# Kernel tuning notes

Measured on AMD Instinct MI355X. Metric: run time of the kernel, lower is better.

## Reference

```python
import jax, jax.numpy as jnp
import numpy as np

NEG_SLOPE = 0.2  # PyG GATv2Conv default negative_slope


def _gatv2_layer(x, src, dst, Wl, Wr, att, bias, heads, out_ch, concat, num_nodes):
    # x: [N, F_in]; src/dst: [E'] (self-loops already appended)
    N, H, C = num_nodes, heads, out_ch
    xl = (x @ Wl).reshape(N, H, C)  # source-side transform (lin_l)
    xr = (x @ Wr).reshape(N, H, C)  # target-side transform (lin_r)
    m = xl[src] + xr[dst]                       # [E', H, C]
    e = jax.nn.leaky_relu(m, NEG_SLOPE)
    logits = jnp.einsum('ehc,hc->eh', e, att)   # [E', H]
    # numerically stable segment softmax over incoming edges of each dst node
    mx = jax.ops.segment_max(logits, dst, num_segments=N)   # [N, H]
    ex = jnp.exp(logits - mx[dst])
    den = jax.ops.segment_sum(ex, dst, num_segments=N)      # [N, H]
    alpha = ex / den[dst]                                    # [E', H]
    out = jax.ops.segment_sum(alpha[:, :, None] * xl[src], dst, num_segments=N)  # [N, H, C]
    out = out.reshape(N, H * C) if concat else out.mean(axis=1)
    return out + bias


def setup_inputs() -> dict:
    key = jax.random.key(0)
    N, E = 50000, 800000
    IN, HID, OUT, HEADS = 128, 32, 64, 4
    ks = jax.random.split(key, 16)
    x = jax.random.normal(ks[0], (N, IN), dtype=jnp.float32)
    edge_index = jax.random.randint(ks[1], (2, E), 0, N, dtype=jnp.int64)

    def lin(k, fin, fout):
        return jax.random.normal(k, (fin, fout), dtype=jnp.float32) * (1.0 / np.sqrt(fin))

    HC = HID * HEADS  # 128
    inp = {
        'x': x, 'edge_index': edge_index,
        # layer 1: IN -> HID x HEADS, concat
        'Wl1': lin(ks[2], IN, HC), 'Wr1': lin(ks[3], IN, HC),
        'a1': jax.random.normal(ks[4], (HEADS, HID), dtype=jnp.float32) * 0.1,
        'b1': jnp.zeros((HC,), dtype=jnp.float32),
        # layer 2: HC -> HID x HEADS, concat
        'Wl2': lin(ks[5], HC, HC), 'Wr2': lin(ks[6], HC, HC),
        'a2': jax.random.normal(ks[7], (HEADS, HID), dtype=jnp.float32) * 0.1,
        'b2': jnp.zeros((HC,), dtype=jnp.float32),
        # layer 3: HC -> OUT, heads=1, concat=False
        'Wl3': lin(ks[8], HC, OUT), 'Wr3': lin(ks[9], HC, OUT),
        'a3': jax.random.normal(ks[10], (1, OUT), dtype=jnp.float32) * 0.1,
        'b3': jnp.zeros((OUT,), dtype=jnp.float32),
    }
    return inp


def reference(x, edge_index, Wl1, Wr1, a1, b1, Wl2, Wr2, a2, b2, Wl3, Wr3, a3, b3):
    N = x.shape[0]
    # PyG GATv2Conv default add_self_loops=True
    loops = jnp.arange(N, dtype=edge_index.dtype)
    src = jnp.concatenate([edge_index[0], loops])
    dst = jnp.concatenate([edge_index[1], loops])
    HID, HEADS, OUT = 32, 4, 64
    h = _gatv2_layer(x, src, dst, Wl1, Wr1, a1, b1, HEADS, HID, True, N)
    h = jax.nn.elu(h)  # eval mode: dropout is identity
    h = _gatv2_layer(h, src, dst, Wl2, Wr2, a2, b2, HEADS, HID, True, N)
    h = jax.nn.elu(h)
    out = _gatv2_layer(h, src, dst, Wl3, Wr3, a3, b3, 1, OUT, False, N)
    return out
```

## Files before the change

kernel.cpp:

```cpp
#include <hip/hip_runtime.h>
#include <cstdint>
#include <cstddef>
#include <math.h>

#define NEG_SLOPE 0.2f
#define DEGB 512
#define EB 4096

typedef unsigned short ushort_t;
typedef __attribute__((ext_vector_type(8))) short short8;
typedef __attribute__((ext_vector_type(4))) float f32x4;
typedef _Float16 half8 __attribute__((ext_vector_type(8)));
typedef _Float16 half2_t __attribute__((ext_vector_type(2)));

__device__ __forceinline__ ushort_t f2bf(float f) {
    unsigned u = __float_as_uint(f);
    unsigned r = u + 0x7FFFu + ((u >> 16) & 1u);
    return (ushort_t)(r >> 16);
}
__device__ __forceinline__ float bf2f(ushort_t h) {
    return __uint_as_float(((unsigned)h) << 16);
}
__device__ __forceinline__ ushort_t f2h(float f) {
    _Float16 h = (_Float16)f;
    return *(ushort_t*)&h;
}

__device__ __forceinline__ float dot2acc(half2_t a, half2_t b, float c) {
#if __has_builtin(__builtin_amdgcn_fdot2)
    return __builtin_amdgcn_fdot2(a, b, c, false);
#else
    return c + (float)a[0] * (float)b[0] + (float)a[1] * (float)b[1];
#endif
}

template<int CTRL>
__device__ __forceinline__ float dpp_add(float p) {
    int t = __builtin_amdgcn_update_dpp(0, __builtin_bit_cast(int, p),
                                        CTRL, 0xF, 0xF, true);
    return p + __builtin_bit_cast(float, t);
}

__device__ __forceinline__ float swz4_add(float p) {
    int t = __builtin_amdgcn_ds_swizzle(__builtin_bit_cast(int, p), 0x101F);
    return p + __builtin_bit_cast(float, t);
}

__device__ __forceinline__ int wave_incl_scan(int v, int lane) {
    #pragma unroll
    for (int o = 1; o < 64; o <<= 1) {
        int t = __shfl_up(v, o, 64);
        if (lane >= o) v += t;
    }
    return v;
}


__global__ void bucket_hist(const int* __restrict__ ei, int E, int Et,
                            int* __restrict__ blkcnt) {
    __shared__ int cnt[256];
    int t = threadIdx.x;
    cnt[t] = 0;
    __syncthreads();
    int e0 = blockIdx.x * EB;
    #pragma unroll
    for (int it = 0; it < EB / 256; ++it) {
        int e = e0 + it * 256 + t;
        if (e < Et) {
            int d = (e < E) ? ei[E + e] : (e - E);
            atomicAdd(&cnt[d >> 8], 1);
        }
    }
    __syncthreads();
    blkcnt[blockIdx.x * 256 + t] = cnt[t];
}

__global__ void colscan(int* __restrict__ blkcnt, int nblk, int* __restrict__ btot) {
    int b = blockIdx.x;
    int lane = threadIdx.x;
    int running = 0;
    for (int base = 0; base < nblk; base += 64) {
        int idx = base + lane;
        int v = (idx < nblk) ? blkcnt[idx * 256 + b] : 0;
        int incl = wave_incl_scan(v, lane);
        if (idx < nblk) blkcnt[idx * 256 + b] = running + incl - v;
        running += __shfl(incl, 63, 64);
    }
    if (lane == 0) btot[b] = running;
}

__global__ void bucketscan(const int* __restrict__ btot, int* __restrict__ bbase) {
    __shared__ int tmp[256];
    int t = threadIdx.x;
    int v = btot[t];
    tmp[t] = v;
    __syncthreads();
    for (int o = 1; o < 256; o <<= 1) {
        int x = (t >= o) ? tmp[t - o] : 0;
        __syncthreads();
        tmp[t] += x;
        __syncthreads();
    }
    bbase[t] = tmp[t] - v;
}

__global__ void bucket_scatter(const int* __restrict__ ei, int E, int Et,
                               const int* __restrict__ blkrel,
                               const int* __restrict__ bbase,
                               unsigned* __restrict__ ebuf) {
    __shared__ int base_l[256];
    __shared__ int cnt[256];
    int t = threadIdx.x;
    base_l[t] = bbase[t] + blkrel[blockIdx.x * 256 + t];
    cnt[t] = 0;
    __syncthreads();
    int e0 = blockIdx.x * EB;
    #pragma unroll
    for (int it = 0; it < EB / 256; ++it) {
        int e = e0 + it * 256 + t;
        if (e < Et) {
            int s, d;
            if (e < E) { s = ei[e]; d = ei[E + e]; }
            else       { s = d = e - E; }
            int b = d >> 8;
            int r = atomicAdd(&cnt[b], 1);
            ebuf[base_l[b] + r] = (unsigned)s | (((unsigned)d & 255u) << 17);
        }
    }
}

__global__ void csr_count(const unsigned* __restrict__ ebuf,
                          const int* __restrict__ bbase,
                          const int* __restrict__ btot,
                          int N, int* __restrict__ deg) {
    __shared__ int dcnt[256];
    int b = blockIdx.x, t = threadIdx.x;
    dcnt[t] = 0;
    __syncthreads();
    int s0 = bbase[b], c = btot[b];
    for (int i = t; i < c; i += 256)
        atomicAdd(&dcnt[ebuf[s0 + i] >> 17], 1);
    __syncthreads();
    int node = b * 256 + t;
    if (node < N) deg[node] = dcnt[t];
}

__global__ void csr_scatter2(const unsigned* __restrict__ ebuf,
                             const int* __restrict__ bbase,
                             const int* __restrict__ btot,
                             const int* __restrict__ rowstart,
                             int N, int* __restrict__ csr_src) {
    __shared__ int cur[256];
    int b = blockIdx.x, t = threadIdx.x;
    int node = b * 256 + t;
    cur[t] = (node < N) ? rowstart[node] : 0;
    __syncthreads();
    int s0 = bbase[b], c = btot[b];
    for (int i = t; i < c; i += 256) {
        unsigned v = ebuf[s0 + i];
        int pos = atomicAdd(&cur[v >> 17], 1);
        csr_src[pos] = (int)(v & 0x1FFFFu);
    }
}

__global__ void scan1(const int* __restrict__ deg, int N,
                      int* __restrict__ excl, int* __restrict__ partials) {
    __shared__ int tmp[256];
    int i = blockIdx.x * 256 + threadIdx.x;
    int v = (i < N) ? deg[i] : 0;
    tmp[threadIdx.x] = v;
    __syncthreads();
    for (int o = 1; o < 256; o <<= 1) {
        int t = (threadIdx.x >= (unsigned)o) ? tmp[threadIdx.x - o] : 0;
        __syncthreads();
        tmp[threadIdx.x] += t;
        __syncthreads();
    }
    if (i < N) excl[i] = tmp[threadIdx.x] - v;
    if (threadIdx.x == 255) partials[blockIdx.x] = tmp[255];
}

__global__ void scan23(int* __restrict__ excl, const int* __restrict__ partials,
                       int nb, int N, int* __restrict__ cursor) {
    __shared__ int tmp[256];
    int t = threadIdx.x;
    tmp[t] = (t < nb) ? partials[t] : 0;
    __syncthreads();
    for (int o = 1; o < 256; o <<= 1) {
        int x = (t >= o) ? tmp[t - o] : 0;
        __syncthreads();
        tmp[t] += x;
        __syncthreads();
    }
    int off = (blockIdx.x > 0) ? tmp[blockIdx.x - 1] : 0;
    int i = blockIdx.x * 256 + t;
    if (i < N) {
        int v = excl[i] + off;
        excl[i] = v;
        cursor[i] = v;
    }
}

__global__ void deg_hist_blk(const int* __restrict__ deg, int N,
                             int* __restrict__ dhist) {
    __shared__ int h[DEGB];
    int t = threadIdx.x;
    for (int b = t; b < DEGB; b += 256) h[b] = 0;
    __syncthreads();
    int i = blockIdx.x * 256 + t;
    if (i < N) {
        int d = deg[i]; if (d > DEGB - 1) d = DEGB - 1;
        atomicAdd(&h[d], 1);
    }
    __syncthreads();
    for (int b = t; b < DEGB; b += 256) {
        int c = h[b];
        if (c) atomicAdd(&dhist[b], c);
    }
}
__global__ void deg_scan(const int* __restrict__ dhist, int* __restrict__ dstart) {
    __shared__ int tmp[DEGB];
    int t = threadIdx.x;
    tmp[t] = dhist[t];
    __syncthreads();
    for (int o = 1; o < DEGB; o <<= 1) {
        int v = (t >= o) ? tmp[t - o] : 0;
        __syncthreads();
        tmp[t] += v;
        __syncthreads();
    }
    int total = tmp[DEGB - 1];
    dstart[t] = total - tmp[t];
}
__global__ void deg_scatter_blk(const int* __restrict__ deg, int N,
                                int* __restrict__ dstart, int* __restrict__ perm) {
    __shared__ int h[DEGB];
    __shared__ int base[DEGB];
    int t = threadIdx.x;
    for (int b = t; b < DEGB; b += 256) h[b] = 0;
    __syncthreads();
    int i = blockIdx.x * 256 + t;
    int d = 0, r = 0;
    if (i < N) {
        d = deg[i]; if (d > DEGB - 1) d = DEGB - 1;
        r = atomicAdd(&h[d], 1);
    }
    __syncthreads();
    for (int b = t; b < DEGB; b += 256) {
        int c = h[b];
        if (c) base[b] = atomicAdd(&dstart[b], c);
    }
    __syncthreads();
    if (i < N) perm[base[d] + r] = i;
}

template<int MOUT, bool CONVA>
__global__ __launch_bounds__(256) void gemm_mfma(const ushort_t* __restrict__ Ah,
                                                 const ushort_t* __restrict__ Al,
                                                 const float* __restrict__ Af,
                                                 const float* __restrict__ Wl,
                                                 const float* __restrict__ Wr,
                                                 ushort_t* __restrict__ xlh,
                                                 ushort_t* __restrict__ xrh, int N) {
    __shared__ __align__(16) ushort_t Bh[8192];
    __shared__ __align__(16) ushort_t Bl[8192];
    const int tid   = threadIdx.x;
    const int row0  = blockIdx.x * 128;
    const int col0v = blockIdx.y * 64;
    const bool isR  = col0v >= MOUT;
    const float* W  = isR ? Wr : Wl;
    const int wcol0 = isR ? (col0v - MOUT) : col0v;
    ushort_t* OUT   = isR ? xrh : xlh;

    #pragma unroll
    for (int i = 0; i < 8; ++i) {
        int idx = tid * 8 + i;
        int k   = idx >> 4;
        int c4  = (idx & 15) * 4;
        float4 w = *(const float4*)(W + (size_t)k * MOUT + wcol0 + c4);
        float wv[4] = {w.x, w.y, w.z, w.w};
        int q = k >> 5, quad = (k >> 3) & 3, j = k & 7;
        #pragma unroll
        for (int e = 0; e < 4; ++e) {
            int c = c4 + e;
            int t = c >> 4;
            int l = (quad << 4) | (c & 15);
            int pos = ((t * 4 + q) * 64 + l) * 8 + j;
            ushort_t hb = f2bf(wv[e]);
            Bh[pos] = hb;
            Bl[pos] = f2bf(wv[e] - bf2f(hb));
        }
    }
    __syncthreads();

    const int wv_  = tid >> 6;
    const int lane = tid & 63;
    const int m    = lane & 15;
    const int quad = lane >> 4;
    const int wrow0 = row0 + wv_ * 32;

    f32x4 acc[2][4] = {};

    for (int q = 0; q < 4; ++q) {
        short8 ahf[2], alf[2];
        #pragma unroll
        for (int r = 0; r < 2; ++r) {
            int row = wrow0 + 16 * r + m;
            row = row < N ? row : N - 1;
            size_t off = (size_t)row * 128 + q * 32 + quad * 8;
            if constexpr (CONVA) {
                float4 f0 = *(const float4*)(Af + off);
                float4 f1 = *(const float4*)(Af + off + 4);
                float fv[8] = {f0.x, f0.y, f0.z, f0.w, f1.x, f1.y, f1.z, f1.w};
                short ah[8], al[8];
                #pragma unroll
                for (int e = 0; e < 8; ++e) {
                    ushort_t hb = f2bf(fv[e]);
                    ah[e] = (short)hb;
                    al[e] = (short)f2bf(fv[e] - bf2f(hb));
                }
                ahf[r] = short8{ah[0],ah[1],ah[2],ah[3],ah[4],ah[5],ah[6],ah[7]};
                alf[r] = short8{al[0],al[1],al[2],al[3],al[4],al[5],al[6],al[7]};
            } else {
                ahf[r] = *(const short8*)(Ah + off);
                alf[r] = *(const short8*)(Al + off);
            }
        }
        #pragma unroll
        for (int t = 0; t < 4; ++t) {
            int base = ((t * 4 + q) * 64 + lane) * 8;
            short8 bh = *(const short8*)(Bh + base);
            short8 bl = *(const short8*)(Bl + base);
            #pragma unroll
            for (int r = 0; r < 2; ++r) {
                acc[r][t] = __builtin_amdgcn_mfma_f32_16x16x32_bf16(ahf[r], bh, acc[r][t], 0, 0, 0);
                acc[r][t] = __builtin_amdgcn_mfma_f32_16x16x32_bf16(ahf[r], bl, acc[r][t], 0, 0, 0);
                acc[r][t] = __builtin_amdgcn_mfma_f32_16x16x32_bf16(alf[r], bh, acc[r][t], 0, 0, 0);
            }
        }
    }

    #pragma unroll
    for (int r = 0; r < 2; ++r)
        #pragma unroll
        for (int i = 0; i < 4; ++i) {
            int row = wrow0 + 16 * r + quad * 4 + i;
            if (row < N) {
                #pragma unroll
                for (int t = 0; t < 4; ++t)
                    OUT[(size_t)row * MOUT + wcol0 + t * 16 + m] = f2h(acc[r][t][i]);
            }
        }
}

template<int H, int C, bool ELU, int OMODE>
__global__ __launch_bounds__(512) void node_attn(const ushort_t* __restrict__ xlh,
                                                 const ushort_t* __restrict__ xrh,
                                                 const float* __restrict__ att,
                                                 const float* __restrict__ bias,
                                                 const int* __restrict__ rowstart,
                                                 const int* __restrict__ deg,
                                                 const int* __restrict__ csr_src,
                                                 const int* __restrict__ perm,
                                                 int N, float* __restrict__ out,
                                                 ushort_t* __restrict__ outh,
                                                 ushort_t* __restrict__ outl) {
    constexpr int HC  = H * C;
    constexpr int VPT = 8;
    constexpr int LPG = HC / VPT;
    constexpr int GPW = 64 / LPG;
    constexpr int GROUP = C / VPT;
    constexpr int DR  = 5;

    const int lane = threadIdx.x & 63;
    const int wv   = threadIdx.x >> 6;
    const int gid  = lane / LPG;
    const int lig  = lane % LPG;
    const int ch0  = lig * VPT;

    const int g0      = (blockIdx.x * 8 + wv) * GPW + gid;
    const int gstride = gridDim.x * 8 * GPW;

    half2_t a2[4];
    {
        float4 u0 = *(const float4*)(att + ch0);
        float4 u1 = *(const float4*)(att + ch0 + 4);
        a2[0] = half2_t{(_Float16)u0.x, (_Float16)u0.y};
        a2[1] = half2_t{(_Float16)u0.z, (_Float16)u0.w};
        a2[2] = half2_t{(_Float16)u1.x, (_Float16)u1.y};
        a2[3] = half2_t{(_Float16)u1.z, (_Float16)u1.w};
    }
    float bias8[VPT];
    {
        float4 b0 = *(const float4*)(bias + ch0);
        float4 b1 = *(const float4*)(bias + ch0 + 4);
        bias8[0]=b0.x; bias8[1]=b0.y; bias8[2]=b0.z; bias8[3]=b0.w;
        bias8[4]=b1.x; bias8[5]=b1.y; bias8[6]=b1.z; bias8[7]=b1.w;
    }
    const half2_t c02 = half2_t{(_Float16)NEG_SLOPE, (_Float16)NEG_SLOPE};

    for (int s = g0; s < N; s += gstride) {
        const int n  = perm[s];
        const int j0 = rowstart[n];
        const int dg = deg[n];

        half8 xrv = *(const half8*)(xrh + (size_t)n * HC + ch0);

        auto ldidx = [&](int e) {
            int ee = e < dg ? e : dg - 1;
            return csr_src[j0 + ee];
        };
        auto ldrow = [&](int idx) -> half8 {
            return *(const half8*)(xlh + (size_t)(unsigned)idx * HC + ch0);
        };

        float d = 0.f;
        float acc[VPT] = {};

        auto process = [&](half8 v) {
            float p = 0.f;
            #pragma unroll
            for (int i = 0; i < 4; ++i) {
                half2_t v2 = half2_t{v[2 * i], v[2 * i + 1]};
                half2_t x2 = half2_t{xrv[2 * i], xrv[2 * i + 1]};
                half2_t m2 = v2 + x2;
                half2_t lr = __builtin_elementwise_max(m2, c02 * m2);
                p = dot2acc(lr, a2[i], p);
            }
            if constexpr (GROUP >= 2) p = dpp_add<0xB1>(p);
            if constexpr (GROUP >= 4) p = dpp_add<0x4E>(p);
            if constexpr (GROUP >= 8) p = swz4_add(p);
            float pe = __expf(p);
            d += pe;
            #pragma unroll
            for (int i = 0; i < VPT; ++i)
                acc[i] += pe * (float)v[i];
        };

        int   ibuf[DR];
        half8 rbuf[DR];
        #pragma unroll
        for (int k = 0; k < DR; ++k) ibuf[k] = ldidx(k);
        #pragma unroll
        for (int k = 0; k < DR; ++k) {
            rbuf[k] = ldrow(ibuf[k]);
            ibuf[k] = ldidx(k + DR);
        }

        int e = 0;
        for (; e + DR <= dg; e += DR) {
            #pragma unroll
            for (int k = 0; k < DR; ++k) {
                half8 v = rbuf[k];
                rbuf[k] = ldrow(ibuf[k]);
                ibuf[k] = ldidx(e + k + 2 * DR);
                process(v);
            }
        }
        #pragma unroll
        for (int k = 0; k < DR; ++k)
            if (e + k < dg) process(rbuf[k]);

        float inv = 1.f / d;
        float vv[VPT];
        #pragma unroll
        for (int i = 0; i < VPT; ++i) {
            float v = acc[i] * inv + bias8[i];
            if (ELU) v = v > 0.f ? v : (__expf(v) - 1.f);
            vv[i] = v;
        }
        if (OMODE == 0) {
            *(float4*)(out + (size_t)n * HC + ch0) =
                make_float4(vv[0], vv[1], vv[2], vv[3]);
            *(float4*)(out + (size_t)n * HC + ch0 + 4) =
                make_float4(vv[4], vv[5], vv[6], vv[7]);
        } else {
            ushort_t hb[VPT], lb[VPT];
            #pragma unroll
            for (int i = 0; i < VPT; ++i) {
                hb[i] = f2bf(vv[i]);
                lb[i] = f2bf(vv[i] - bf2f(hb[i]));
            }
            *(ushort4*)(outh + (size_t)n * HC + ch0) =
                ushort4{hb[0], hb[1], hb[2], hb[3]};
            *(ushort4*)(outh + (size_t)n * HC + ch0 + 4) =
                ushort4{hb[4], hb[5], hb[6], hb[7]};
            *(ushort4*)(outl + (size_t)n * HC + ch0) =
                ushort4{lb[0], lb[1], lb[2], lb[3]};
            *(ushort4*)(outl + (size_t)n * HC + ch0 + 4) =
                ushort4{lb[4], lb[5], lb[6], lb[7]};
        }
    }
}

extern "C" void kernel_launch(void* const* d_in, const int* in_sizes, int n_in,
                              void* d_out, int out_size, void* d_ws, size_t ws_size,
                              hipStream_t stream) {
    const float* x   = (const float*)d_in[0];
    const int*   ei  = (const int*)d_in[1];
    const float* Wl1 = (const float*)d_in[2];
    const float* Wr1 = (const float*)d_in[3];
    const float* a1  = (const float*)d_in[4];
    const float* b1  = (const float*)d_in[5];
    const float* Wl2 = (const float*)d_in[6];
    const float* Wr2 = (const float*)d_in[7];
    const float* a2  = (const float*)d_in[8];
    const float* b2  = (const float*)d_in[9];
    const float* Wl3 = (const float*)d_in[10];
    const float* Wr3 = (const float*)d_in[11];
    const float* a3  = (const float*)d_in[12];
    const float* b3  = (const float*)d_in[13];

    const int N  = in_sizes[0] / 128;
    const int E  = in_sizes[1] / 2;
    const int Et = E + N;
    const int nb = (N + 255) / 256;

    char* p = (char*)d_ws;
    auto alloc = [&](size_t bytes) -> void* {
        void* r = (void*)p;
        p += (bytes + 255) & ~(size_t)255;
        return r;
    };
    const int ebBlocks = (Et + EB - 1) / EB;
    int*      csr_src  = (int*)alloc((size_t)Et * 4 + 256);
    unsigned* ebuf     = (unsigned*)alloc((size_t)Et * 4);
    int*      blkcnt   = (int*)alloc((size_t)ebBlocks * 256 * 4);
    int*      btot     = (int*)alloc(256 * 4);
    int*      bbase    = (int*)alloc(256 * 4);
    int*      deg      = (int*)alloc((size_t)N * 4);
    int*      rowstart = (int*)alloc((size_t)N * 4);
    int*      cursor   = (int*)alloc((size_t)N * 4);
    int*      partials = (int*)alloc((size_t)nb * 4);
    int*      perm     = (int*)alloc((size_t)N * 4);
    int*      dhist    = (int*)alloc((size_t)DEGB * 4);
    int*      dstart   = (int*)alloc((size_t)DEGB * 4);
    ushort_t* xlh      = (ushort_t*)alloc((size_t)N * 128 * 2);
    ushort_t* xrh      = (ushort_t*)alloc((size_t)N * 128 * 2);
    ushort_t* Ah       = (ushort_t*)alloc((size_t)N * 128 * 2);
    ushort_t* Al       = (ushort_t*)alloc((size_t)N * 128 * 2);

    const int rowBlocks   = (N + 127) / 128;
    const int nodeBlocks12 = (N + 31) / 32;
    const int nodeBlocks3  = (N + 63) / 64;

    hipMemsetAsync(dhist, 0, (size_t)DEGB * 4, stream);
    bucket_hist<<<ebBlocks, 256, 0, stream>>>(ei, E, Et, blkcnt);
    colscan<<<256, 64, 0, stream>>>(blkcnt, ebBlocks, btot);
    bucketscan<<<1, 256, 0, stream>>>(btot, bbase);
    bucket_scatter<<<ebBlocks, 256, 0, stream>>>(ei, E, Et, blkcnt, bbase, ebuf);
    csr_count<<<nb, 256, 0, stream>>>(ebuf, bbase, btot, N, deg);
    scan1<<<nb, 256, 0, stream>>>(deg, N, rowstart, partials);
    scan23<<<nb, 256, 0, stream>>>(rowstart, partials, nb, N, cursor);
    csr_scatter2<<<nb, 256, 0, stream>>>(ebuf, bbase, btot, rowstart, N, csr_src);
    deg_hist_blk<<<nb, 256, 0, stream>>>(deg, N, dhist);
    deg_scan<<<1, DEGB, 0, stream>>>(dhist, dstart);
    deg_scatter_blk<<<nb, 256, 0, stream>>>(deg, N, dstart, perm);

    gemm_mfma<128, true><<<dim3(rowBlocks, 4), 256, 0, stream>>>(
        nullptr, nullptr, x, Wl1, Wr1, xlh, xrh, N);
    node_attn<4, 32, true, 1><<<nodeBlocks12, 512, 0, stream>>>(
        xlh, xrh, a1, b1, rowstart, deg, csr_src, perm, N, nullptr, Ah, Al);

    gemm_mfma<128, false><<<dim3(rowBlocks, 4), 256, 0, stream>>>(
        Ah, Al, nullptr, Wl2, Wr2, xlh, xrh, N);
    node_attn<4, 32, true, 1><<<nodeBlocks12, 512, 0, stream>>>(
        xlh, xrh, a2, b2, rowstart, deg, csr_src, perm, N, nullptr, Ah, Al);

    float* out = (float*)d_out;
    gemm_mfma<64, false><<<dim3(rowBlocks, 2), 256, 0, stream>>>(
        Ah, Al, nullptr, Wl3, Wr3, xlh, xrh, N);
    node_attn<1, 64, false, 0><<<nodeBlocks3, 512, 0, stream>>>(
        xlh, xrh, a3, b3, rowstart, deg, csr_src, perm, N, out, nullptr, nullptr);
}
```

Measured before the change: 309.5 us.

## Fuse CSR and degree-sort preprocessing into one persistent kernel with grid barriers

Eleven small preprocessing kernels (bucket histogram, scans, scatters, CSR count and scatter, degree sort) are merged into a single kernel that uses atomic-counter grid barriers between phases. Count, scan, and degree-histogram steps now share one phase, and the unused cursor buffer is dropped. The aim is to remove per-launch overhead and the gaps between many tiny dependent kernels. The cost is that correctness depends on all blocks (ebBlocks, about 208 with 256 threads) being co-resident, or the spin barrier deadlocks, and phases where few blocks have work now block the whole grid.

```diff
diff --git a/kernel.cpp b/kernel.cpp
--- a/kernel.cpp
+++ b/kernel.cpp
@@ -56,202 +56,183 @@
 }
 
 
-__global__ void bucket_hist(const int* __restrict__ ei, int E, int Et,
-                            int* __restrict__ blkcnt) {
-    __shared__ int cnt[256];
-    int t = threadIdx.x;
-    cnt[t] = 0;
+__device__ __forceinline__ void gbar(int* __restrict__ bar, int ph, int nblk) {
     __syncthreads();
-    int e0 = blockIdx.x * EB;
-    #pragma unroll
-    for (int it = 0; it < EB / 256; ++it) {
-        int e = e0 + it * 256 + t;
-        if (e < Et) {
-            int d = (e < E) ? ei[E + e] : (e - E);
-            atomicAdd(&cnt[d >> 8], 1);
-        }
+    if (threadIdx.x == 0) {
+        __threadfence();
+        atomicAdd(&bar[ph], 1);
+        while (__hip_atomic_load(&bar[ph], __ATOMIC_RELAXED,
+                                 __HIP_MEMORY_SCOPE_AGENT) < nblk) {}
     }
     __syncthreads();
-    blkcnt[blockIdx.x * 256 + t] = cnt[t];
-}
-
-__global__ void colscan(int* __restrict__ blkcnt, int nblk, int* __restrict__ btot) {
-    int b = blockIdx.x;
-    int lane = threadIdx.x;
-    int running = 0;
-    for (int base = 0; base < nblk; base += 64) {
-        int idx = base + lane;
-        int v = (idx < nblk) ? blkcnt[idx * 256 + b] : 0;
-        int incl = wave_incl_scan(v, lane);
-        if (idx < nblk) blkcnt[idx * 256 + b] = running + incl - v;
-        running += __shfl(incl, 63, 64);
-    }
-    if (lane == 0) btot[b] = running;
-}
-
-__global__ void bucketscan(const int* __restrict__ btot, int* __restrict__ bbase) {
-    __shared__ int tmp[256];
-    int t = threadIdx.x;
-    int v = btot[t];
-    tmp[t] = v;
+    __threadfence();
+}
+
+__global__ __launch_bounds__(256) void build_all(
+        const int* __restrict__ ei, int E, int Et, int N, int nbkt,
+        int* __restrict__ blkcnt, int* __restrict__ btot, int* __restrict__ bbase,
+        unsigned* __restrict__ ebuf,
+        int* __restrict__ deg, int* __restrict__ rowstart, int* __restrict__ partials,
+        int* __restrict__ dhist, int* __restrict__ dstart, int* __restrict__ perm,
+        int* __restrict__ csr_src, int* __restrict__ bar) {
+    __shared__ int sA[256];
+    __shared__ int sB[256];
+    __shared__ int sC[512];
+    __shared__ int sD[512];
+    const int t    = threadIdx.x;
+    const int blk  = blockIdx.x;
+    const int nblk = gridDim.x;
+
+    sA[t] = 0;
     __syncthreads();
-    for (int o = 1; o < 256; o <<= 1) {
-        int x = (t >= o) ? tmp[t - o] : 0;
-        __syncthreads();
-        tmp[t] += x;
-        __syncthreads();
-    }
-    bbase[t] = tmp[t] - v;
-}
-
-__global__ void bucket_scatter(const int* __restrict__ ei, int E, int Et,
-                               const int* __restrict__ blkrel,
-                               const int* __restrict__ bbase,
-                               unsigned* __restrict__ ebuf) {
-    __shared__ int base_l[256];
-    __shared__ int cnt[256];
-    int t = threadIdx.x;
-    base_l[t] = bbase[t] + blkrel[blockIdx.x * 256 + t];
-    cnt[t] = 0;
-    __syncthreads();
-    int e0 = blockIdx.x * EB;
-    #pragma unroll
-    for (int it = 0; it < EB / 256; ++it) {
-        int e = e0 + it * 256 + t;
-        if (e < Et) {
-            int s, d;
-            if (e < E) { s = ei[e]; d = ei[E + e]; }
-            else       { s = d = e - E; }
-            int b = d >> 8;
-            int r = atomicAdd(&cnt[b], 1);
-            ebuf[base_l[b] + r] = (unsigned)s | (((unsigned)d & 255u) << 17);
-        }
-    }
-}
-
-__global__ void csr_count(const unsigned* __restrict__ ebuf,
-                          const int* __restrict__ bbase,
-                          const int* __restrict__ btot,
-                          int N, int* __restrict__ deg) {
-    __shared__ int dcnt[256];
-    int b = blockIdx.x, t = threadIdx.x;
-    dcnt[t] = 0;
-    __syncthreads();
-    int s0 = bbase[b], c = btot[b];
-    for (int i = t; i < c; i += 256)
-        atomicAdd(&dcnt[ebuf[s0 + i] >> 17], 1);
-    __syncthreads();
-    int node = b * 256 + t;
-    if (node < N) deg[node] = dcnt[t];
-}
-
-__global__ void csr_scatter2(const unsigned* __restrict__ ebuf,
-                             const int* __restrict__ bbase,
-                             const int* __restrict__ btot,
-                             const int* __restrict__ rowstart,
-                             int N, int* __restrict__ csr_src) {
-    __shared__ int cur[256];
-    int b = blockIdx.x, t = threadIdx.x;
-    int node = b * 256 + t;
-    cur[t] = (node < N) ? rowstart[node] : 0;
-    __syncthreads();
-    int s0 = bbase[b], c = btot[b];
-    for (int i = t; i < c; i += 256) {
-        unsigned v = ebuf[s0 + i];
-        int pos = atomicAdd(&cur[v >> 17], 1);
-        csr_src[pos] = (int)(v & 0x1FFFFu);
-    }
-}
-
-__global__ void scan1(const int* __restrict__ deg, int N,
-                      int* __restrict__ excl, int* __restrict__ partials) {
-    __shared__ int tmp[256];
-    int i = blockIdx.x * 256 + threadIdx.x;
-    int v = (i < N) ? deg[i] : 0;
-    tmp[threadIdx.x] = v;
-    __syncthreads();
-    for (int o = 1; o < 256; o <<= 1) {
-        int t = (threadIdx.x >= (unsigned)o) ? tmp[threadIdx.x - o] : 0;
-        __syncthreads();
-        tmp[threadIdx.x] += t;
-        __syncthreads();
-    }
-    if (i < N) excl[i] = tmp[threadIdx.x] - v;
-    if (threadIdx.x == 255) partials[blockIdx.x] = tmp[255];
-}
-
-__global__ void scan23(int* __restrict__ excl, const int* __restrict__ partials,
-                       int nb, int N, int* __restrict__ cursor) {
-    __shared__ int tmp[256];
-    int t = threadIdx.x;
-    tmp[t] = (t < nb) ? partials[t] : 0;
-    __syncthreads();
-    for (int o = 1; o < 256; o <<= 1) {
-        int x = (t >= o) ? tmp[t - o] : 0;
-        __syncthreads();
-        tmp[t] += x;
-        __syncthreads();
-    }
-    int off = (blockIdx.x > 0) ? tmp[blockIdx.x - 1] : 0;
-    int i = blockIdx.x * 256 + t;
-    if (i < N) {
-        int v = excl[i] + off;
-        excl[i] = v;
-        cursor[i] = v;
-    }
-}
-
-__global__ void deg_hist_blk(const int* __restrict__ deg, int N,
-                             int* __restrict__ dhist) {
-    __shared__ int h[DEGB];
-    int t = threadIdx.x;
-    for (int b = t; b < DEGB; b += 256) h[b] = 0;
-    __syncthreads();
-    int i = blockIdx.x * 256 + t;
-    if (i < N) {
-        int d = deg[i]; if (d > DEGB - 1) d = DEGB - 1;
-        atomicAdd(&h[d], 1);
-    }
-    __syncthreads();
-    for (int b = t; b < DEGB; b += 256) {
-        int c = h[b];
-        if (c) atomicAdd(&dhist[b], c);
-    }
-}
-__global__ void deg_scan(const int* __restrict__ dhist, int* __restrict__ dstart) {
-    __shared__ int tmp[DEGB];
-    int t = threadIdx.x;
-    tmp[t] = dhist[t];
-    __syncthreads();
-    for (int o = 1; o < DEGB; o <<= 1) {
-        int v = (t >= o) ? tmp[t - o] : 0;
-        __syncthreads();
-        tmp[t] += v;
-        __syncthreads();
-    }
-    int total = tmp[DEGB - 1];
-    dstart[t] = total - tmp[t];
-}
-__global__ void deg_scatter_blk(const int* __restrict__ deg, int N,
-                                int* __restrict__ dstart, int* __restrict__ perm) {
-    __shared__ int h[DEGB];
-    __shared__ int base[DEGB];
-    int t = threadIdx.x;
-    for (int b = t; b < DEGB; b += 256) h[b] = 0;
-    __syncthreads();
-    int i = blockIdx.x * 256 + t;
-    int d = 0, r = 0;
-    if (i < N) {
-        d = deg[i]; if (d > DEGB - 1) d = DEGB - 1;
-        r = atomicAdd(&h[d], 1);
-    }
-    __syncthreads();
-    for (int b = t; b < DEGB; b += 256) {
-        int c = h[b];
-        if (c) base[b] = atomicAdd(&dstart[b], c);
-    }
-    __syncthreads();
-    if (i < N) perm[base[d] + r] = i;
+    {
+        int e0 = blk * EB;
+        #pragma unroll
+        for (int it = 0; it < EB / 256; ++it) {
+            int e = e0 + it * 256 + t;
+            if (e < Et) {
+                int d = (e < E) ? ei[E + e] : (e - E);
+                atomicAdd(&sA[d >> 8], 1);
+            }
+        }
+        __syncthreads();
+        blkcnt[blk * 256 + t] = sA[t];
+    }
+    gbar(bar, 0, nblk);
+
+    for (int b = blk; b < 256; b += nblk) {
+        if (t < 64) {
+            int lane = t;
+            int running = 0;
+            for (int base = 0; base < nblk; base += 64) {
+                int idx = base + lane;
+                int v = (idx < nblk) ? blkcnt[idx * 256 + b] : 0;
+                int incl = wave_incl_scan(v, lane);
+                if (idx < nblk) blkcnt[idx * 256 + b] = running + incl - v;
+                running += __shfl(incl, 63, 64);
+            }
+            if (lane == 0) btot[b] = running;
+        }
+    }
+    gbar(bar, 1, nblk);
+
+    if (blk == 0) {
+        int v = btot[t];
+        sB[t] = v;
+        __syncthreads();
+        for (int o = 1; o < 256; o <<= 1) {
+            int x = (t >= o) ? sB[t - o] : 0;
+            __syncthreads();
+            sB[t] += x;
+            __syncthreads();
+        }
+        bbase[t] = sB[t] - v;
+    }
+    gbar(bar, 2, nblk);
+
+    {
+        sA[t] = bbase[t] + blkcnt[blk * 256 + t];
+        sB[t] = 0;
+        __syncthreads();
+        int e0 = blk * EB;
+        #pragma unroll
+        for (int it = 0; it < EB / 256; ++it) {
+            int e = e0 + it * 256 + t;
+            if (e < Et) {
+                int s, d;
+                if (e < E) { s = ei[e]; d = ei[E + e]; }
+                else       { s = d = e - E; }
+                int b = d >> 8;
+                int r = atomicAdd(&sB[b], 1);
+                ebuf[sA[b] + r] = (unsigned)s | (((unsigned)d & 255u) << 17);
+            }
+        }
+    }
+    gbar(bar, 3, nblk);
+
+    int rs_excl = 0;
+    if (blk < nbkt) {
+        sA[t] = 0;
+        sC[t] = 0; sC[t + 256] = 0;
+        __syncthreads();
+        int s0 = bbase[blk], c = btot[blk];
+        for (int i = t; i < c; i += 256)
+            atomicAdd(&sA[ebuf[s0 + i] >> 17], 1);
+        __syncthreads();
+        int node = blk * 256 + t;
+        int dv = sA[t];
+        if (node < N) deg[node] = dv;
+        sB[t] = dv;
+        __syncthreads();
+        for (int o = 1; o < 256; o <<= 1) {
+            int x = (t >= o) ? sB[t - o] : 0;
+            __syncthreads();
+            sB[t] += x;
+            __syncthreads();
+        }
+        rs_excl = sB[t] - dv;
+        if (t == 255) partials[blk] = sB[255];
+        if (node < N) {
+            int dc = dv < DEGB - 1 ? dv : DEGB - 1;
+            atomicAdd(&sC[dc], 1);
+        }
+        __syncthreads();
+        int c0 = sC[t];       if (c0) atomicAdd(&dhist[t], c0);
+        int c1 = sC[t + 256]; if (c1) atomicAdd(&dhist[t + 256], c1);
+    }
+    gbar(bar, 4, nblk);
+
+    if (blk < nbkt) {
+        sB[t] = (t < nbkt) ? partials[t] : 0;
+        __syncthreads();
+        for (int o = 1; o < 256; o <<= 1) {
+            int x = (t >= o) ? sB[t - o] : 0;
+            __syncthreads();
+            sB[t] += x;
+            __syncthreads();
+        }
+        int off = (blk > 0) ? sB[blk - 1] : 0;
+        int node = blk * 256 + t;
+        if (node < N) rowstart[node] = rs_excl + off;
+    } else if (blk == nbkt) {
+        sC[t]       = dhist[t];
+        sC[t + 256] = dhist[t + 256];
+        __syncthreads();
+        for (int o = 1; o < 512; o <<= 1) {
+            int v0 = (t >= o) ? sC[t - o] : 0;
+            int v1 = (t + 256 >= o) ? sC[t + 256 - o] : 0;
+            __syncthreads();
+            sC[t] += v0;
+            sC[t + 256] += v1;
+            __syncthreads();
+        }
+        int total = sC[511];
+        dstart[t]       = total - sC[t];
+        dstart[t + 256] = total - sC[t + 256];
+    }
+    gbar(bar, 5, nblk);
+
+    if (blk < nbkt) {
+        int node = blk * 256 + t;
+        sB[t] = (node < N) ? rowstart[node] : 0;
+        sC[t] = 0; sC[t + 256] = 0;
+        __syncthreads();
+        int s0 = bbase[blk], c = btot[blk];
+        for (int i = t; i < c; i += 256) {
+            unsigned v = ebuf[s0 + i];
+            int pos = atomicAdd(&sB[v >> 17], 1);
+            csr_src[pos] = (int)(v & 0x1FFFFu);
+        }
+        int dv = sA[t];
+        int dc = dv < DEGB - 1 ? dv : DEGB - 1;
+        int r = 0;
+        if (node < N) r = atomicAdd(&sC[dc], 1);
+        __syncthreads();
+        int c0 = sC[t];       if (c0) sD[t]       = atomicAdd(&dstart[t], c0);
+        int c1 = sC[t + 256]; if (c1) sD[t + 256] = atomicAdd(&dstart[t + 256], c1);
+        __syncthreads();
+        if (node < N) perm[sD[dc] + r] = node;
+    }
 }
 
 template<int MOUT, bool CONVA>
@@ -530,10 +511,10 @@
     int*      bbase    = (int*)alloc(256 * 4);
     int*      deg      = (int*)alloc((size_t)N * 4);
     int*      rowstart = (int*)alloc((size_t)N * 4);
-    int*      cursor   = (int*)alloc((size_t)N * 4);
     int*      partials = (int*)alloc((size_t)nb * 4);
     int*      perm     = (int*)alloc((size_t)N * 4);
     int*      dhist    = (int*)alloc((size_t)DEGB * 4);
+    int*      bar      = (int*)alloc(64 * 4);
     int*      dstart   = (int*)alloc((size_t)DEGB * 4);
     ushort_t* xlh      = (ushort_t*)alloc((size_t)N * 128 * 2);
     ushort_t* xrh      = (ushort_t*)alloc((size_t)N * 128 * 2);
@@ -544,18 +525,10 @@
     const int nodeBlocks12 = (N + 31) / 32;
     const int nodeBlocks3  = (N + 63) / 64;
 
-    hipMemsetAsync(dhist, 0, (size_t)DEGB * 4, stream);
-    bucket_hist<<<ebBlocks, 256, 0, stream>>>(ei, E, Et, blkcnt);
-    colscan<<<256, 64, 0, stream>>>(blkcnt, ebBlocks, btot);
-    bucketscan<<<1, 256, 0, stream>>>(btot, bbase);
-    bucket_scatter<<<ebBlocks, 256, 0, stream>>>(ei, E, Et, blkcnt, bbase, ebuf);
-    csr_count<<<nb, 256, 0, stream>>>(ebuf, bbase, btot, N, deg);
-    scan1<<<nb, 256, 0, stream>>>(deg, N, rowstart, partials);
-    scan23<<<nb, 256, 0, stream>>>(rowstart, partials, nb, N, cursor);
-    csr_scatter2<<<nb, 256, 0, stream>>>(ebuf, bbase, btot, rowstart, N, csr_src);
-    deg_hist_blk<<<nb, 256, 0, stream>>>(deg, N, dhist);
-    deg_scan<<<1, DEGB, 0, stream>>>(dhist, dstart);
-    deg_scatter_blk<<<nb, 256, 0, stream>>>(deg, N, dstart, perm);
+    hipMemsetAsync(dhist, 0, (size_t)DEGB * 4 + 64 * 4, stream);
+    build_all<<<ebBlocks, 256, 0, stream>>>(
+        ei, E, Et, N, nb, blkcnt, btot, bbase, ebuf,
+        deg, rowstart, partials, dhist, dstart, perm, csr_src, bar);
 
     gemm_mfma<128, true><<<dim3(rowBlocks, 4), 256, 0, stream>>>(
         nullptr, nullptr, x, Wl1, Wr1, xlh, xrh, N);
```

After: 423.2 us. +36.7%, slower.

## Pack node descriptors and prefetch next node's descriptor and xr row

Applied to the files above, without the earlier changes.

Replaces the perm/rowstart/deg triple of dependent loads with a single packed int4 descriptor per degree-sorted node, built in the degree scatter kernel. The attention kernel now prefetches the next node's descriptor and its target-side feature row while the current node is being processed, hiding that pointer-chasing latency. The node kernel grids are also halved, so each group handles two nodes and the prefetch has something to overlap with. The cost is a larger descriptor array and fewer resident groups.

```diff
diff --git a/kernel.cpp b/kernel.cpp
--- a/kernel.cpp
+++ b/kernel.cpp
@@ -232,18 +232,20 @@
     int total = tmp[DEGB - 1];
     dstart[t] = total - tmp[t];
 }
-__global__ void deg_scatter_blk(const int* __restrict__ deg, int N,
-                                int* __restrict__ dstart, int* __restrict__ perm) {
+__global__ void deg_scatter_blk(const int* __restrict__ deg,
+                                const int* __restrict__ rowstart, int N,
+                                int* __restrict__ dstart, int4* __restrict__ desc) {
     __shared__ int h[DEGB];
     __shared__ int base[DEGB];
     int t = threadIdx.x;
     for (int b = t; b < DEGB; b += 256) h[b] = 0;
     __syncthreads();
     int i = blockIdx.x * 256 + t;
-    int d = 0, r = 0;
+    int dv = 0, dc = 0, r = 0;
     if (i < N) {
-        d = deg[i]; if (d > DEGB - 1) d = DEGB - 1;
-        r = atomicAdd(&h[d], 1);
+        dv = deg[i];
+        dc = dv < DEGB - 1 ? dv : DEGB - 1;
+        r = atomicAdd(&h[dc], 1);
     }
     __syncthreads();
     for (int b = t; b < DEGB; b += 256) {
@@ -251,7 +253,7 @@
         if (c) base[b] = atomicAdd(&dstart[b], c);
     }
     __syncthreads();
-    if (i < N) perm[base[d] + r] = i;
+    if (i < N) desc[base[dc] + r] = make_int4(i, rowstart[i], dv, 0);
 }
 
 template<int MOUT, bool CONVA>
@@ -358,10 +360,8 @@
                                                  const ushort_t* __restrict__ xrh,
                                                  const float* __restrict__ att,
                                                  const float* __restrict__ bias,
-                                                 const int* __restrict__ rowstart,
-                                                 const int* __restrict__ deg,
+                                                 const int4* __restrict__ desc,
                                                  const int* __restrict__ csr_src,
-                                                 const int* __restrict__ perm,
                                                  int N, float* __restrict__ out,
                                                  ushort_t* __restrict__ outh,
                                                  ushort_t* __restrict__ outl) {
@@ -399,12 +399,18 @@
     }
     const half2_t c02 = half2_t{(_Float16)NEG_SLOPE, (_Float16)NEG_SLOPE};
 
+    if (g0 >= N) return;
+
+    int4  dsc = desc[g0];
+    half8 xrv = *(const half8*)(xrh + (size_t)dsc.x * HC + ch0);
+
     for (int s = g0; s < N; s += gstride) {
-        const int n  = perm[s];
-        const int j0 = rowstart[n];
-        const int dg = deg[n];
-
-        half8 xrv = *(const half8*)(xrh + (size_t)n * HC + ch0);
+        const int n  = dsc.x;
+        const int j0 = dsc.y;
+        const int dg = dsc.z;
+
+        const int s2 = s + gstride;
+        const int4 dsc2 = desc[s2 < N ? s2 : s];
 
         auto ldidx = [&](int e) {
             int ee = e < dg ? e : dg - 1;
@@ -460,6 +466,8 @@
         #pragma unroll
         for (int k = 0; k < DR; ++k)
             if (e + k < dg) process(rbuf[k]);
+
+        half8 xrv2 = *(const half8*)(xrh + (size_t)dsc2.x * HC + ch0);
 
         float inv = 1.f / d;
         float vv[VPT];
@@ -490,6 +498,9 @@
             *(ushort4*)(outl + (size_t)n * HC + ch0 + 4) =
                 ushort4{lb[4], lb[5], lb[6], lb[7]};
         }
+
+        dsc = dsc2;
+        xrv = xrv2;
     }
 }
 
@@ -532,7 +543,7 @@
     int*      rowstart = (int*)alloc((size_t)N * 4);
     int*      cursor   = (int*)alloc((size_t)N * 4);
     int*      partials = (int*)alloc((size_t)nb * 4);
-    int*      perm     = (int*)alloc((size_t)N * 4);
+    int4*     desc     = (int4*)alloc((size_t)N * 16);
     int*      dhist    = (int*)alloc((size_t)DEGB * 4);
     int*      dstart   = (int*)alloc((size_t)DEGB * 4);
     ushort_t* xlh      = (ushort_t*)alloc((size_t)N * 128 * 2);
@@ -540,9 +551,9 @@
     ushort_t* Ah       = (ushort_t*)alloc((size_t)N * 128 * 2);
     ushort_t* Al       = (ushort_t*)alloc((size_t)N * 128 * 2);
 
-    const int rowBlocks   = (N + 127) / 128;
-    const int nodeBlocks12 = (N + 31) / 32;
-    const int nodeBlocks3  = (N + 63) / 64;
+    const int rowBlocks    = (N + 127) / 128;
+    const int nodeBlocks12 = (N + 63) / 64;
+    const int nodeBlocks3  = (N + 127) / 128;
 
     hipMemsetAsync(dhist, 0, (size_t)DEGB * 4, stream);
     bucket_hist<<<ebBlocks, 256, 0, stream>>>(ei, E, Et, blkcnt);
@@ -555,21 +566,21 @@
     csr_scatter2<<<nb, 256, 0, stream>>>(ebuf, bbase, btot, rowstart, N, csr_src);
     deg_hist_blk<<<nb, 256, 0, stream>>>(deg, N, dhist);
     deg_scan<<<1, DEGB, 0, stream>>>(dhist, dstart);
-    deg_scatter_blk<<<nb, 256, 0, stream>>>(deg, N, dstart, perm);
+    deg_scatter_blk<<<nb, 256, 0, stream>>>(deg, rowstart, N, dstart, desc);
 
     gemm_mfma<128, true><<<dim3(rowBlocks, 4), 256, 0, stream>>>(
         nullptr, nullptr, x, Wl1, Wr1, xlh, xrh, N);
     node_attn<4, 32, true, 1><<<nodeBlocks12, 512, 0, stream>>>(
-        xlh, xrh, a1, b1, rowstart, deg, csr_src, perm, N, nullptr, Ah, Al);
+        xlh, xrh, a1, b1, desc, csr_src, N, nullptr, Ah, Al);
 
     gemm_mfma<128, false><<<dim3(rowBlocks, 4), 256, 0, stream>>>(
         Ah, Al, nullptr, Wl2, Wr2, xlh, xrh, N);
     node_attn<4, 32, true, 1><<<nodeBlocks12, 512, 0, stream>>>(
-        xlh, xrh, a2, b2, rowstart, deg, csr_src, perm, N, nullptr, Ah, Al);
+        xlh, xrh, a2, b2, desc, csr_src, N, nullptr, Ah, Al);
 
     float* out = (float*)d_out;
     gemm_mfma<64, false><<<dim3(rowBlocks, 2), 256, 0, stream>>>(
         Ah, Al, nullptr, Wl3, Wr3, xlh, xrh, N);
     node_attn<1, 64, false, 0><<<nodeBlocks3, 512, 0, stream>>>(
-        xlh, xrh, a3, b3, rowstart, deg, csr_src, perm, N, out, nullptr, nullptr);
-}
+        xlh, xrh, a3, b3, desc, csr_src, N, out, nullptr, nullptr);
+}
```

New measurement: 315.1 us. Within noise of the previous version (+1.8%).
